# Performance work log

Measured on AMD Instinct MI355X. Metric: run time of the kernel, lower is better.

The kernel has to match this reference:

```python
import jax, jax.numpy as jnp
import numpy as np

N, D, K = 16384, 256, 4096   # tokens, feature dim, codebook_size
GAMMA = 0.99


def setup_inputs() -> dict:
    key = jax.random.key(0)
    k1, k2, k3 = jax.random.split(key, 3)
    features = jax.random.normal(k1, (N, D), dtype=jnp.float32)
    mask = jax.random.uniform(k2, (N,)) < 0.9
    codebook = jax.random.normal(k3, (K, D), dtype=jnp.float32)  # hk RandomNormal init
    count = jnp.zeros((K,), jnp.float32)
    avg = jnp.zeros((K,), jnp.float32)
    return {"features": features, "mask": mask, "codebook": codebook,
            "count": count, "avg": avg}


def reference(features, mask, codebook, count, avg):
    sg = jax.lax.stop_gradient
    prev_codebook = codebook

    # pairwise squared distances [N, K] via ||f||^2 - 2 f.C^T + ||c||^2
    f2 = jnp.sum(features * features, axis=-1)            # [N]
    c2 = jnp.sum(codebook * codebook, axis=-1)            # [K]
    distance = f2[:, None] - 2.0 * (features @ codebook.T) + c2[None, :]
    distance = jnp.where(mask[:, None], distance, jnp.inf)

    assign_fwd = jnp.argmin(distance, axis=1)             # [N] nearest code per token
    assign_rev = jnp.argmin(distance, axis=0)             # [K] nearest token per code
    features_fwd = codebook[assign_fwd]                   # [N, D]
    features_rev = features[assign_rev]                   # [K, D]

    # straight-through estimator
    out_features = sg(features_fwd) + features - sg(features)

    total = jnp.maximum(mask.sum(), 1).astype(features.dtype)
    commitment = jnp.mean((sg(features_fwd) - features) ** 2, axis=-1)
    commitment_loss = jnp.where(mask, commitment, 0.0).sum() / total

    # scatter-add assignment counts (masked) and feature sums (unmasked, as in source)
    assignment_count = jnp.zeros((K,), jnp.float32).at[assign_fwd].add(
        mask.astype(jnp.float32))
    assignment_mask = assignment_count < 1

    count = (1.0 - GAMMA) * assignment_count + GAMMA * count
    avg = (1.0 - GAMMA) * assignment_count / total + GAMMA * avg
    alpha = jnp.exp(-avg * K * 10.0 / (1.0 - GAMMA) - 0.001)

    feat_sum = jnp.zeros_like(codebook).at[assign_fwd].add(features)  # [K, D]
    assigned_update = (GAMMA * codebook + (1.0 - GAMMA) * feat_sum)
    assigned_update = assigned_update / jnp.maximum(count[:, None], 1.0)
    unassigned_update = (1.0 - alpha)[:, None] * codebook + alpha[:, None] * features_rev
    new_codebook = jnp.where(assignment_mask[:, None], assigned_update, unassigned_update)

    # pmean(delta) is identity on a single device; final = prev + (prev - new), as in source
    codebook_delta = prev_codebook - new_codebook
    new_codebook = prev_codebook + codebook_delta

    unassigned_percent = (assignment_count > 0).mean()
    return (out_features, assign_fwd, commitment_loss, unassigned_percent,
            count, avg, new_codebook)
```

## Files before the change

### kernel.cpp

```cpp
#include <hip/hip_runtime.h>
#include <math.h>

typedef unsigned long long u64;
typedef unsigned int u32;

#define N_TOK 16384
#define DIM   256
#define KCB   4096

#define WS_ROWMIN   0
#define WS_COLMIN   131072
#define WS_CNT      163840
#define WS_CPART    180224
#define WS_TOTAL    181248
#define WS_FLAG     181252
#define WS_F2       181312
#define WS_C2       246848
#define WS_END      263232

#define OUT_FEAT    0
#define OUT_ASSIGN  4194304
#define OUT_CLOSS   4210688
#define OUT_UPCT    4210689
#define OUT_COUNT   4210690
#define OUT_AVG     4214786
#define OUT_CB      4218882

#define C_1MG 0.009999999776482582f

__device__ __forceinline__ u32 fkey(float d) {
    u32 u = __float_as_uint(d);
    return (u & 0x80000000u) ? ~u : (u | 0x80000000u);
}
__device__ __forceinline__ u64 u64min(u64 a, u64 b) { return a < b ? a : b; }
__device__ __forceinline__ u64 shflxor64(u64 v, int m) {
    int lo = __shfl_xor((int)(u32)(v & 0xFFFFFFFFULL), m, 64);
    int hi = __shfl_xor((int)(u32)(v >> 32), m, 64);
    return ((u64)(u32)hi << 32) | (u32)lo;
}
__device__ __forceinline__ bool read_mask(const void* mp, int flag, int n) {
    if (flag == 2) return ((const float*)mp)[n] != 0.0f;
    if (flag == 1) return ((const int*)mp)[n] != 0;
    return ((const unsigned char*)mp)[n] != 0;
}

__global__ void k_detect(const void* __restrict__ mp, int* __restrict__ flag) {
    if (threadIdx.x == 0) {
        const u32* w = (const u32*)mp;
        bool allf = true, alli = true, any1 = false;
        for (int i = 0; i < 64; ++i) {
            u32 x = w[i];
            if (x != 0u && x != 0x3F800000u) allf = false;
            if (x == 0x3F800000u) any1 = true;
            if (x > 1u) alli = false;
        }
        *flag = (allf && any1) ? 2 : (alli ? 1 : 0);
    }
}

__global__ __launch_bounds__(256)
void k_norms(const float* __restrict__ F, const float* __restrict__ CB,
             const void* __restrict__ mp, const int* __restrict__ flagp,
             float* __restrict__ f2, float* __restrict__ c2) {
    __shared__ float red[4];
    const int b = blockIdx.x, d = threadIdx.x;
    const float* src = (b < N_TOK) ? (F + (size_t)b * DIM) : (CB + (size_t)(b - N_TOK) * DIM);
    float v = src[d];
    float s = v * v;
#pragma unroll
    for (int m = 32; m > 0; m >>= 1) s += __shfl_xor(s, m, 64);
    if ((d & 63) == 0) red[d >> 6] = s;
    __syncthreads();
    if (d == 0) {
        float tot = red[0] + red[1] + red[2] + red[3];
        if (b < N_TOK) {
            bool msk = read_mask(mp, *flagp, b);
            f2[b] = msk ? tot : __builtin_huge_valf();
        } else {
            c2[b - N_TOK] = tot;
        }
    }
}

__global__ __launch_bounds__(256, 4)
void k_gemm(const float* __restrict__ F, const float* __restrict__ CB,
            const float* __restrict__ f2, const float* __restrict__ c2,
            u64* __restrict__ rowmin, u64* __restrict__ colmin) {
    __shared__ float As[128][32];
    __shared__ float Bs[128][32];
    __shared__ u64 colred[4][128];

    const int t = threadIdx.x;
    const int ty = t >> 4, tx = t & 15;
    const int wave = t >> 6;
    const int rowbase = blockIdx.x * 128;
    const int kbase = blockIdx.y * 128;

    float acc[8][8];
#pragma unroll
    for (int i = 0; i < 8; ++i)
#pragma unroll
        for (int j = 0; j < 8; ++j) acc[i][j] = 0.0f;

    for (int dc = 0; dc < 8; ++dc) {
        const int db = dc * 32;
#pragma unroll
        for (int i = 0; i < 4; ++i) {
            int g = t + i * 256;
            int r = g >> 3;
            int c4 = (g & 7) << 2;
            int sw = c4 ^ (((r >> 3) & 7) << 2);
            *(float4*)&As[r][sw] = *(const float4*)(F + (size_t)(rowbase + r) * DIM + db + c4);
            *(float4*)&Bs[r][sw] = *(const float4*)(CB + (size_t)(kbase + r) * DIM + db + c4);
        }
        __syncthreads();
#pragma unroll
        for (int dd = 0; dd < 32; dd += 2) {
            float2 a[8], b[8];
#pragma unroll
            for (int i = 0; i < 8; ++i)
                a[i] = *(const float2*)&As[ty * 8 + i][dd ^ ((ty & 7) << 2)];
#pragma unroll
            for (int j = 0; j < 8; ++j)
                b[j] = *(const float2*)&Bs[tx * 8 + j][dd ^ ((tx & 7) << 2)];
#pragma unroll
            for (int i = 0; i < 8; ++i)
#pragma unroll
                for (int j = 0; j < 8; ++j) {
                    acc[i][j] = fmaf(a[i].x, b[j].x, acc[i][j]);
                    acc[i][j] = fmaf(a[i].y, b[j].y, acc[i][j]);
                }
        }
        __syncthreads();
    }

    float c2k[8];
#pragma unroll
    for (int j = 0; j < 8; ++j) c2k[j] = c2[kbase + tx * 8 + j];
    u64 cbst[8];
#pragma unroll
    for (int j = 0; j < 8; ++j) cbst[j] = ~0ULL;

#pragma unroll
    for (int i = 0; i < 8; ++i) {
        const int row = rowbase + ty * 8 + i;
        const float f2r = f2[row];
        u64 rbst = ~0ULL;
#pragma unroll
        for (int j = 0; j < 8; ++j) {
            float dist = (f2r - 2.0f * acc[i][j]) + c2k[j];
            u64 hk = (u64)fkey(dist) << 32;
            rbst    = u64min(rbst, hk | (u32)(kbase + tx * 8 + j));
            cbst[j] = u64min(cbst[j], hk | (u32)row);
        }
        rbst = u64min(rbst, shflxor64(rbst, 1));
        rbst = u64min(rbst, shflxor64(rbst, 2));
        rbst = u64min(rbst, shflxor64(rbst, 4));
        rbst = u64min(rbst, shflxor64(rbst, 8));
        if (tx == 0) atomicMin(&rowmin[row], rbst);
    }

#pragma unroll
    for (int j = 0; j < 8; ++j) {
        cbst[j] = u64min(cbst[j], shflxor64(cbst[j], 16));
        cbst[j] = u64min(cbst[j], shflxor64(cbst[j], 32));
    }
    if ((t & 63) < 16) {
#pragma unroll
        for (int j = 0; j < 8; ++j) colred[wave][tx * 8 + j] = cbst[j];
    }
    __syncthreads();
    if (t < 128) {
        u64 m = u64min(u64min(colred[0][t], colred[1][t]),
                       u64min(colred[2][t], colred[3][t]));
        atomicMin(&colmin[kbase + t], m);
    }
}

__global__ __launch_bounds__(256)
void k_token(const float* __restrict__ F, const float* __restrict__ CB,
             const u64* __restrict__ rowmin, const void* __restrict__ mp,
             const int* __restrict__ flagp,
             float* __restrict__ out_feat, float* __restrict__ out_assign,
             float* __restrict__ cnt, float* __restrict__ fsum,
             float* __restrict__ cpart) {
    __shared__ float red[4];
    const int n = blockIdx.x, d = threadIdx.x;
    const int k = (int)(u32)(rowmin[n] & 0xFFFFFFFFULL);
    const float f = F[(size_t)n * DIM + d];
    const float cv = CB[(size_t)k * DIM + d];
    out_feat[(size_t)n * DIM + d] = (cv + f) - f;
    const float df = cv - f;
    float s = df * df;
#pragma unroll
    for (int m = 32; m > 0; m >>= 1) s += __shfl_xor(s, m, 64);
    if ((d & 63) == 0) red[d >> 6] = s;
    __syncthreads();
    atomicAdd(&fsum[(size_t)k * DIM + d], f);
    if (d == 0) {
        out_assign[n] = (float)k;
        bool msk = read_mask(mp, *flagp, n);
        if (msk) {
            float tot = red[0] + red[1] + red[2] + red[3];
            atomicAdd(&cnt[k], 1.0f);
            atomicAdd(&cpart[n & 255], tot * (1.0f / 256.0f));
        }
    }
}

__global__ __launch_bounds__(256)
void k_scalars(const float* __restrict__ cnt, const float* __restrict__ cpart,
               float* __restrict__ totf, float* __restrict__ out) {
    __shared__ float redf[4], redc[4];
    __shared__ int redi[4];
    const int t = threadIdx.x;
    float ts = 0.0f;
    int asg = 0;
    for (int i = t; i < KCB; i += 256) {
        float v = cnt[i];
        ts += v;
        asg += (v > 0.0f) ? 1 : 0;
    }
    float cs = cpart[t];
#pragma unroll
    for (int m = 32; m > 0; m >>= 1) {
        ts += __shfl_xor(ts, m, 64);
        cs += __shfl_xor(cs, m, 64);
        asg += __shfl_xor(asg, m, 64);
    }
    if ((t & 63) == 0) { redf[t >> 6] = ts; redc[t >> 6] = cs; redi[t >> 6] = asg; }
    __syncthreads();
    if (t == 0) {
        float total = redf[0] + redf[1] + redf[2] + redf[3];
        total = fmaxf(total, 1.0f);
        float closs = (redc[0] + redc[1] + redc[2] + redc[3]) / total;
        int a = redi[0] + redi[1] + redi[2] + redi[3];
        totf[0] = total;
        out[OUT_CLOSS] = closs;
        out[OUT_UPCT] = (float)a / 4096.0f;
    }
}

__global__ __launch_bounds__(256)
void k_cbupd(const float* __restrict__ F, const float* __restrict__ CB,
             const float* __restrict__ cnt_in, const float* __restrict__ avg_in,
             const float* __restrict__ ac_, const float* __restrict__ fsum,
             const u64* __restrict__ colmin, const float* __restrict__ totf,
             float* __restrict__ out_count, float* __restrict__ out_avg,
             float* __restrict__ out_cb) {
    const int k = blockIdx.x, d = threadIdx.x;
    const float ac = ac_[k];
    const float total = totf[0];
    const float cn = C_1MG * ac + 0.99f * cnt_in[k];
    const float av = (C_1MG * ac) / total + 0.99f * avg_in[k];
    const float arg = ((-av * 4096.0f) * 10.0f) / C_1MG - 0.001f;
    const float alpha = expf(arg);
    const int tok = (int)(u32)(colmin[k] & 0xFFFFFFFFULL);
    const float cb = CB[(size_t)k * DIM + d];
    const float fs = fsum[(size_t)k * DIM + d];
    const float fr = F[(size_t)tok * DIM + d];
    const float assigned = (0.99f * cb + C_1MG * fs) / fmaxf(cn, 1.0f);
    const float unass = (1.0f - alpha) * cb + alpha * fr;
    const float nc = (ac < 1.0f) ? assigned : unass;
    out_cb[(size_t)k * DIM + d] = cb + (cb - nc);
    if (d == 0) { out_count[k] = cn; out_avg[k] = av; }
}

extern "C" void kernel_launch(void* const* d_in, const int* in_sizes, int n_in,
                              void* d_out, int out_size, void* d_ws, size_t ws_size,
                              hipStream_t stream) {
    const float* F   = (const float*)d_in[0];
    const void*  Mp  = d_in[1];
    const float* CB  = (const float*)d_in[2];
    const float* CNT = (const float*)d_in[3];
    const float* AVG = (const float*)d_in[4];
    float* out = (float*)d_out;
    char* ws = (char*)d_ws;
    if (ws_size < (size_t)WS_END) return;

    u64*   rowmin = (u64*)(ws + WS_ROWMIN);
    u64*   colmin = (u64*)(ws + WS_COLMIN);
    float* cnt    = (float*)(ws + WS_CNT);
    float* cpart  = (float*)(ws + WS_CPART);
    float* totf   = (float*)(ws + WS_TOTAL);
    int*   flag   = (int*)(ws + WS_FLAG);
    float* f2     = (float*)(ws + WS_F2);
    float* c2     = (float*)(ws + WS_C2);
    float* fsum   = out + OUT_CB;

    hipMemsetAsync(ws, 0xFF, 163840, stream);
    hipMemsetAsync(ws + WS_CNT, 0, WS_FLAG - WS_CNT, stream);
    hipMemsetAsync(fsum, 0, (size_t)KCB * DIM * sizeof(float), stream);

    k_detect<<<1, 64, 0, stream>>>(Mp, flag);
    k_norms<<<N_TOK + KCB, 256, 0, stream>>>(F, CB, Mp, flag, f2, c2);
    k_gemm<<<dim3(128, 32), 256, 0, stream>>>(F, CB, f2, c2, rowmin, colmin);
    k_token<<<N_TOK, 256, 0, stream>>>(F, CB, rowmin, Mp, flag,
                                       out + OUT_FEAT, out + OUT_ASSIGN,
                                       cnt, fsum, cpart);
    k_scalars<<<1, 256, 0, stream>>>(cnt, cpart, totf, out);
    k_cbupd<<<KCB, 256, 0, stream>>>(F, CB, CNT, AVG, cnt, fsum, colmin, totf,
                                     out + OUT_COUNT, out + OUT_AVG, out + OUT_CB);
}
```

Before: 639.5 us.

## Use direct global-to-LDS loads and 512-thread blocks in distance GEMM

The FP32 distance GEMM now stages its A and B tiles with global_load_lds, which writes straight into shared memory and skips the round trip through registers. Blocks grow from 256 to 512 threads, so each thread accumulates a 4x8 tile instead of 8x8. This cuts register pressure, and the column-min reduction now spans 8 waves. The price is lower per-thread compute intensity and more LDS reads per FMA, and the swizzle layout has to match the fixed per-wave LDS placement that global_load_lds uses.

```diff
diff --git a/kernel.cpp b/kernel.cpp
--- a/kernel.cpp
+++ b/kernel.cpp
@@ -42,6 +42,11 @@
     if (flag == 2) return ((const float*)mp)[n] != 0.0f;
     if (flag == 1) return ((const int*)mp)[n] != 0;
     return ((const unsigned char*)mp)[n] != 0;
+}
+__device__ __forceinline__ void gload_lds16(const float* g, void* l) {
+    __builtin_amdgcn_global_load_lds((const __attribute__((address_space(1))) void*)g,
+                                     (__attribute__((address_space(3))) void*)l,
+                                     16, 0, 0);
 }
 
 __global__ void k_detect(const void* __restrict__ mp, int* __restrict__ flag) {
@@ -82,49 +87,60 @@
     }
 }
 
-__global__ __launch_bounds__(256, 4)
+__global__ __launch_bounds__(512, 2)
 void k_gemm(const float* __restrict__ F, const float* __restrict__ CB,
             const float* __restrict__ f2, const float* __restrict__ c2,
             u64* __restrict__ rowmin, u64* __restrict__ colmin) {
     __shared__ float As[128][32];
     __shared__ float Bs[128][32];
-    __shared__ u64 colred[4][128];
+    __shared__ u64 colred[8][128];
 
     const int t = threadIdx.x;
-    const int ty = t >> 4, tx = t & 15;
+    const int tx = t & 15;
+    const int ty = t >> 4;
     const int wave = t >> 6;
     const int rowbase = blockIdx.x * 128;
     const int kbase = blockIdx.y * 128;
 
-    float acc[8][8];
-#pragma unroll
-    for (int i = 0; i < 8; ++i)
+    const int g0 = t, g1 = 512 + t;
+    const int r0 = g0 >> 3;
+    const int r1 = g1 >> 3;
+    const int c0 = ((g0 & 7) << 2) ^ (((g0 >> 6) & 7) << 2);
+    const int c1 = ((g1 & 7) << 2) ^ (((g1 >> 6) & 7) << 2);
+    const float* Fb = F + (size_t)rowbase * DIM;
+    const float* Cb = CB + (size_t)kbase * DIM;
+    char* AsB = (char*)As;
+    char* BsB = (char*)Bs;
+    const int ldsA0 = wave * 1024;
+    const int ldsA1 = 8192 + wave * 1024;
+
+    float acc[4][8];
+#pragma unroll
+    for (int i = 0; i < 4; ++i)
 #pragma unroll
         for (int j = 0; j < 8; ++j) acc[i][j] = 0.0f;
+
+    const int aswz = ((ty >> 1) & 7) << 2;
+    const int bswz = (tx & 7) << 2;
 
     for (int dc = 0; dc < 8; ++dc) {
         const int db = dc * 32;
-#pragma unroll
-        for (int i = 0; i < 4; ++i) {
-            int g = t + i * 256;
-            int r = g >> 3;
-            int c4 = (g & 7) << 2;
-            int sw = c4 ^ (((r >> 3) & 7) << 2);
-            *(float4*)&As[r][sw] = *(const float4*)(F + (size_t)(rowbase + r) * DIM + db + c4);
-            *(float4*)&Bs[r][sw] = *(const float4*)(CB + (size_t)(kbase + r) * DIM + db + c4);
-        }
+        gload_lds16(Fb + (size_t)r0 * DIM + db + c0, AsB + ldsA0);
+        gload_lds16(Fb + (size_t)r1 * DIM + db + c1, AsB + ldsA1);
+        gload_lds16(Cb + (size_t)r0 * DIM + db + c0, BsB + ldsA0);
+        gload_lds16(Cb + (size_t)r1 * DIM + db + c1, BsB + ldsA1);
         __syncthreads();
 #pragma unroll
         for (int dd = 0; dd < 32; dd += 2) {
-            float2 a[8], b[8];
-#pragma unroll
-            for (int i = 0; i < 8; ++i)
-                a[i] = *(const float2*)&As[ty * 8 + i][dd ^ ((ty & 7) << 2)];
+            float2 a[4], b[8];
+#pragma unroll
+            for (int i = 0; i < 4; ++i)
+                a[i] = *(const float2*)&As[ty * 4 + i][dd ^ aswz];
 #pragma unroll
             for (int j = 0; j < 8; ++j)
-                b[j] = *(const float2*)&Bs[tx * 8 + j][dd ^ ((tx & 7) << 2)];
-#pragma unroll
-            for (int i = 0; i < 8; ++i)
+                b[j] = *(const float2*)&Bs[tx * 8 + j][dd ^ bswz];
+#pragma unroll
+            for (int i = 0; i < 4; ++i)
 #pragma unroll
                 for (int j = 0; j < 8; ++j) {
                     acc[i][j] = fmaf(a[i].x, b[j].x, acc[i][j]);
@@ -142,8 +158,8 @@
     for (int j = 0; j < 8; ++j) cbst[j] = ~0ULL;
 
 #pragma unroll
-    for (int i = 0; i < 8; ++i) {
-        const int row = rowbase + ty * 8 + i;
+    for (int i = 0; i < 4; ++i) {
+        const int row = rowbase + ty * 4 + i;
         const float f2r = f2[row];
         u64 rbst = ~0ULL;
 #pragma unroll
@@ -171,8 +187,9 @@
     }
     __syncthreads();
     if (t < 128) {
-        u64 m = u64min(u64min(colred[0][t], colred[1][t]),
-                       u64min(colred[2][t], colred[3][t]));
+        u64 m = colred[0][t];
+#pragma unroll
+        for (int w = 1; w < 8; ++w) m = u64min(m, colred[w][t]);
         atomicMin(&colmin[kbase + t], m);
     }
 }
@@ -294,7 +311,7 @@
 
     k_detect<<<1, 64, 0, stream>>>(Mp, flag);
     k_norms<<<N_TOK + KCB, 256, 0, stream>>>(F, CB, Mp, flag, f2, c2);
-    k_gemm<<<dim3(128, 32), 256, 0, stream>>>(F, CB, f2, c2, rowmin, colmin);
+    k_gemm<<<dim3(128, 32), 512, 0, stream>>>(F, CB, f2, c2, rowmin, colmin);
     k_token<<<N_TOK, 256, 0, stream>>>(F, CB, rowmin, Mp, flag,
                                        out + OUT_FEAT, out + OUT_ASSIGN,
                                        cnt, fsum, cpart);
```

New measurement: 597.1 us. 6.6% less time.

## Use 512-thread GEMM blocks with 4x8 strided microtiles and padded LDS

Applied to the files above, without the earlier changes.

The distance GEMM now runs with 512 threads per 128x128 tile. Each thread computes a 4x8 strided microtile instead of 8x8, and LDS reads become float4 over a 36-float padded row instead of the XOR swizzle. The column-min reduction buffer now reuses the As shared array and reduces across 8 waves. The aim is more waves for latency hiding, fewer LDS instructions and less shared memory. In exchange each thread does less arithmetic per LDS load, and the strided row/column mapping changes the access pattern.

```diff
diff --git a/kernel.cpp b/kernel.cpp
--- a/kernel.cpp
+++ b/kernel.cpp
@@ -82,75 +82,88 @@
     }
 }
 
-__global__ __launch_bounds__(256, 4)
+__global__ __launch_bounds__(512, 2)
 void k_gemm(const float* __restrict__ F, const float* __restrict__ CB,
             const float* __restrict__ f2, const float* __restrict__ c2,
             u64* __restrict__ rowmin, u64* __restrict__ colmin) {
-    __shared__ float As[128][32];
-    __shared__ float Bs[128][32];
-    __shared__ u64 colred[4][128];
+    __shared__ float As[128][36];
+    __shared__ float Bs[128][36];
 
     const int t = threadIdx.x;
-    const int ty = t >> 4, tx = t & 15;
+    const int tx = t & 15;
+    const int ty = t >> 4;
     const int wave = t >> 6;
     const int rowbase = blockIdx.x * 128;
     const int kbase = blockIdx.y * 128;
 
-    float acc[8][8];
-#pragma unroll
-    for (int i = 0; i < 8; ++i)
+    const int r0 = t >> 3, c0 = (t & 7) << 2;
+    const int r1 = (512 + t) >> 3, c1 = c0;
+
+    float acc[4][8];
+#pragma unroll
+    for (int i = 0; i < 4; ++i)
 #pragma unroll
         for (int j = 0; j < 8; ++j) acc[i][j] = 0.0f;
+
+    const float* aB[4];
+    const float* bB[8];
+#pragma unroll
+    for (int i = 0; i < 4; ++i) aB[i] = &As[ty + i * 32][0];
+#pragma unroll
+    for (int j = 0; j < 8; ++j) bB[j] = &Bs[tx + j * 16][0];
 
     for (int dc = 0; dc < 8; ++dc) {
         const int db = dc * 32;
-#pragma unroll
-        for (int i = 0; i < 4; ++i) {
-            int g = t + i * 256;
-            int r = g >> 3;
-            int c4 = (g & 7) << 2;
-            int sw = c4 ^ (((r >> 3) & 7) << 2);
-            *(float4*)&As[r][sw] = *(const float4*)(F + (size_t)(rowbase + r) * DIM + db + c4);
-            *(float4*)&Bs[r][sw] = *(const float4*)(CB + (size_t)(kbase + r) * DIM + db + c4);
+        {
+            float4 va0 = *(const float4*)(F + (size_t)(rowbase + r0) * DIM + db + c0);
+            float4 vb0 = *(const float4*)(CB + (size_t)(kbase + r0) * DIM + db + c0);
+            float4 va1 = *(const float4*)(F + (size_t)(rowbase + r1) * DIM + db + c1);
+            float4 vb1 = *(const float4*)(CB + (size_t)(kbase + r1) * DIM + db + c1);
+            *(float4*)&As[r0][c0] = va0;
+            *(float4*)&Bs[r0][c0] = vb0;
+            *(float4*)&As[r1][c1] = va1;
+            *(float4*)&Bs[r1][c1] = vb1;
         }
         __syncthreads();
 #pragma unroll
-        for (int dd = 0; dd < 32; dd += 2) {
-            float2 a[8], b[8];
-#pragma unroll
-            for (int i = 0; i < 8; ++i)
-                a[i] = *(const float2*)&As[ty * 8 + i][dd ^ ((ty & 7) << 2)];
-#pragma unroll
-            for (int j = 0; j < 8; ++j)
-                b[j] = *(const float2*)&Bs[tx * 8 + j][dd ^ ((tx & 7) << 2)];
-#pragma unroll
-            for (int i = 0; i < 8; ++i)
+        for (int dd = 0; dd < 32; dd += 4) {
+            float4 a[4], b[8];
+#pragma unroll
+            for (int i = 0; i < 4; ++i) a[i] = *(const float4*)(aB[i] + dd);
+#pragma unroll
+            for (int j = 0; j < 8; ++j) b[j] = *(const float4*)(bB[j] + dd);
+#pragma unroll
+            for (int i = 0; i < 4; ++i)
 #pragma unroll
                 for (int j = 0; j < 8; ++j) {
                     acc[i][j] = fmaf(a[i].x, b[j].x, acc[i][j]);
                     acc[i][j] = fmaf(a[i].y, b[j].y, acc[i][j]);
+                    acc[i][j] = fmaf(a[i].z, b[j].z, acc[i][j]);
+                    acc[i][j] = fmaf(a[i].w, b[j].w, acc[i][j]);
                 }
         }
         __syncthreads();
     }
 
+    u64* colred = (u64*)&As[0][0];
+
     float c2k[8];
 #pragma unroll
-    for (int j = 0; j < 8; ++j) c2k[j] = c2[kbase + tx * 8 + j];
+    for (int j = 0; j < 8; ++j) c2k[j] = c2[kbase + tx + j * 16];
     u64 cbst[8];
 #pragma unroll
     for (int j = 0; j < 8; ++j) cbst[j] = ~0ULL;
 
 #pragma unroll
-    for (int i = 0; i < 8; ++i) {
-        const int row = rowbase + ty * 8 + i;
+    for (int i = 0; i < 4; ++i) {
+        const int row = rowbase + ty + i * 32;
         const float f2r = f2[row];
         u64 rbst = ~0ULL;
 #pragma unroll
         for (int j = 0; j < 8; ++j) {
             float dist = (f2r - 2.0f * acc[i][j]) + c2k[j];
             u64 hk = (u64)fkey(dist) << 32;
-            rbst    = u64min(rbst, hk | (u32)(kbase + tx * 8 + j));
+            rbst    = u64min(rbst, hk | (u32)(kbase + tx + j * 16));
             cbst[j] = u64min(cbst[j], hk | (u32)row);
         }
         rbst = u64min(rbst, shflxor64(rbst, 1));
@@ -167,12 +180,13 @@
     }
     if ((t & 63) < 16) {
 #pragma unroll
-        for (int j = 0; j < 8; ++j) colred[wave][tx * 8 + j] = cbst[j];
+        for (int j = 0; j < 8; ++j) colred[wave * 128 + tx + j * 16] = cbst[j];
     }
     __syncthreads();
     if (t < 128) {
-        u64 m = u64min(u64min(colred[0][t], colred[1][t]),
-                       u64min(colred[2][t], colred[3][t]));
+        u64 m = colred[t];
+#pragma unroll
+        for (int w = 1; w < 8; ++w) m = u64min(m, colred[w * 128 + t]);
         atomicMin(&colmin[kbase + t], m);
     }
 }
@@ -294,7 +308,7 @@
 
     k_detect<<<1, 64, 0, stream>>>(Mp, flag);
     k_norms<<<N_TOK + KCB, 256, 0, stream>>>(F, CB, Mp, flag, f2, c2);
-    k_gemm<<<dim3(128, 32), 256, 0, stream>>>(F, CB, f2, c2, rowmin, colmin);
+    k_gemm<<<dim3(128, 32), 512, 0, stream>>>(F, CB, f2, c2, rowmin, colmin);
     k_token<<<N_TOK, 256, 0, stream>>>(F, CB, rowmin, Mp, flag,
                                        out + OUT_FEAT, out + OUT_ASSIGN,
                                        cnt, fsum, cpart);
```

Result: slower. 823.0 us (+28.7%).

## Read feature tile directly from global memory and stage only codebook in LDS

Applied to the files above, without the earlier changes.

The GEMM kernel no longer stages the feature tile in shared memory. Each thread now loads its eight feature rows straight from global memory (through cache) as float4, and only the codebook tile goes to LDS, in 64-wide padded chunks. Thread-to-row/column mapping changes to strided (ty + i*16, tx + j*16), and the launch-bounds occupancy hint is dropped. This halves LDS traffic and barriers per chunk, but adds uncoalesced per-thread global loads of feature rows and may raise register pressure.

```diff
diff --git a/kernel.cpp b/kernel.cpp
--- a/kernel.cpp
+++ b/kernel.cpp
@@ -82,16 +82,16 @@
     }
 }
 
-__global__ __launch_bounds__(256, 4)
+__global__ __launch_bounds__(256)
 void k_gemm(const float* __restrict__ F, const float* __restrict__ CB,
             const float* __restrict__ f2, const float* __restrict__ c2,
             u64* __restrict__ rowmin, u64* __restrict__ colmin) {
-    __shared__ float As[128][32];
-    __shared__ float Bs[128][32];
+    __shared__ float Bs[128][68];
     __shared__ u64 colred[4][128];
 
     const int t = threadIdx.x;
-    const int ty = t >> 4, tx = t & 15;
+    const int tx = t & 15;
+    const int ty = t >> 4;
     const int wave = t >> 6;
     const int rowbase = blockIdx.x * 128;
     const int kbase = blockIdx.y * 128;
@@ -102,55 +102,57 @@
 #pragma unroll
         for (int j = 0; j < 8; ++j) acc[i][j] = 0.0f;
 
-    for (int dc = 0; dc < 8; ++dc) {
-        const int db = dc * 32;
-#pragma unroll
-        for (int i = 0; i < 4; ++i) {
-            int g = t + i * 256;
-            int r = g >> 3;
-            int c4 = (g & 7) << 2;
-            int sw = c4 ^ (((r >> 3) & 7) << 2);
-            *(float4*)&As[r][sw] = *(const float4*)(F + (size_t)(rowbase + r) * DIM + db + c4);
-            *(float4*)&Bs[r][sw] = *(const float4*)(CB + (size_t)(kbase + r) * DIM + db + c4);
-        }
+    const float* aP[8];
+#pragma unroll
+    for (int i = 0; i < 8; ++i) aP[i] = F + (size_t)(rowbase + ty + i * 16) * DIM;
+
+    for (int ch = 0; ch < 4; ++ch) {
         __syncthreads();
 #pragma unroll
-        for (int dd = 0; dd < 32; dd += 2) {
-            float2 a[8], b[8];
-#pragma unroll
-            for (int i = 0; i < 8; ++i)
-                a[i] = *(const float2*)&As[ty * 8 + i][dd ^ ((ty & 7) << 2)];
-#pragma unroll
-            for (int j = 0; j < 8; ++j)
-                b[j] = *(const float2*)&Bs[tx * 8 + j][dd ^ ((tx & 7) << 2)];
+        for (int p = 0; p < 8; ++p) {
+            const int idx = t + p * 256;
+            const int r = idx >> 4;
+            const int c4 = (idx & 15) << 2;
+            *(float4*)&Bs[r][c4] =
+                *(const float4*)(CB + (size_t)(kbase + r) * DIM + ch * 64 + c4);
+        }
+        __syncthreads();
+#pragma unroll
+        for (int dd = 0; dd < 64; dd += 4) {
+            float4 a[8], b[8];
+#pragma unroll
+            for (int i = 0; i < 8; ++i) a[i] = *(const float4*)(aP[i] + ch * 64 + dd);
+#pragma unroll
+            for (int j = 0; j < 8; ++j) b[j] = *(const float4*)&Bs[tx + j * 16][dd];
 #pragma unroll
             for (int i = 0; i < 8; ++i)
 #pragma unroll
                 for (int j = 0; j < 8; ++j) {
                     acc[i][j] = fmaf(a[i].x, b[j].x, acc[i][j]);
                     acc[i][j] = fmaf(a[i].y, b[j].y, acc[i][j]);
+                    acc[i][j] = fmaf(a[i].z, b[j].z, acc[i][j]);
+                    acc[i][j] = fmaf(a[i].w, b[j].w, acc[i][j]);
                 }
         }
-        __syncthreads();
     }
 
     float c2k[8];
 #pragma unroll
-    for (int j = 0; j < 8; ++j) c2k[j] = c2[kbase + tx * 8 + j];
+    for (int j = 0; j < 8; ++j) c2k[j] = c2[kbase + tx + j * 16];
     u64 cbst[8];
 #pragma unroll
     for (int j = 0; j < 8; ++j) cbst[j] = ~0ULL;
 
 #pragma unroll
     for (int i = 0; i < 8; ++i) {
-        const int row = rowbase + ty * 8 + i;
+        const int row = rowbase + ty + i * 16;
         const float f2r = f2[row];
         u64 rbst = ~0ULL;
 #pragma unroll
         for (int j = 0; j < 8; ++j) {
             float dist = (f2r - 2.0f * acc[i][j]) + c2k[j];
             u64 hk = (u64)fkey(dist) << 32;
-            rbst    = u64min(rbst, hk | (u32)(kbase + tx * 8 + j));
+            rbst    = u64min(rbst, hk | (u32)(kbase + tx + j * 16));
             cbst[j] = u64min(cbst[j], hk | (u32)row);
         }
         rbst = u64min(rbst, shflxor64(rbst, 1));
@@ -165,9 +167,10 @@
         cbst[j] = u64min(cbst[j], shflxor64(cbst[j], 16));
         cbst[j] = u64min(cbst[j], shflxor64(cbst[j], 32));
     }
+    __syncthreads();
     if ((t & 63) < 16) {
 #pragma unroll
-        for (int j = 0; j < 8; ++j) colred[wave][tx * 8 + j] = cbst[j];
+        for (int j = 0; j < 8; ++j) colred[wave][tx + j * 16] = cbst[j];
     }
     __syncthreads();
     if (t < 128) {
```

Result: slower. 1.055 ms (+65.0%).
